# Optimization experiments

Hardware: AMD Instinct MI355X
Metric: run time of the kernel (lower is better)

Reference implementation:

```python
import jax, jax.numpy as jnp
import numpy as np

H = 12        # attention heads
BETA = 0.5    # blend weight between ctx-cosine probs and QK probs
LN_EPS = 1e-12


def layer_norm(x, g, b):
    mu = x.mean(-1, keepdims=True)
    var = ((x - mu) ** 2).mean(-1, keepdims=True)
    return (x - mu) * jax.lax.rsqrt(var + LN_EPS) * g + b


def setup_inputs() -> dict:
    key = jax.random.key(0)
    B, S, D, F, L = 16, 512, 768, 3072, 4
    ks = jax.random.split(key, 9)
    w = lambda k, shape: (jax.random.normal(k, shape, jnp.float32) * 0.02)
    return {
        "hidden_states": jax.random.normal(ks[0], (B, S, D), jnp.float32),
        "Wq": w(ks[1], (L, D, D)), "bq": jnp.zeros((L, D), jnp.float32),
        "Wk": w(ks[2], (L, D, D)), "bk": jnp.zeros((L, D), jnp.float32),
        "Wv": w(ks[3], (L, D, D)), "bv": jnp.zeros((L, D), jnp.float32),
        "Wc": w(ks[4], (L, D, D)), "bc": jnp.zeros((L, D), jnp.float32),
        "Wo": w(ks[5], (L, D, D)), "bo": jnp.zeros((L, D), jnp.float32),
        "g1": jnp.ones((L, D), jnp.float32), "b1": jnp.zeros((L, D), jnp.float32),
        "Wi": w(ks[6], (L, D, F)), "bi": jnp.zeros((L, F), jnp.float32),
        "Wo2": w(ks[7], (L, F, D)), "bo2": jnp.zeros((L, D), jnp.float32),
        "g2": jnp.ones((L, D), jnp.float32), "b2": jnp.zeros((L, D), jnp.float32),
    }


def reference(hidden_states, Wq, bq, Wk, bk, Wv, bv, Wc, bc, Wo, bo,
              g1, b1, Wi, bi, Wo2, bo2, g2, b2):
    B, S, D = hidden_states.shape
    Dh = D // H
    L = Wq.shape[0]
    eye = jnp.eye(S, dtype=hidden_states.dtype)
    scale = 1.0 / np.sqrt(Dh).astype(np.float32)

    def heads(t):  # [B,S,D] -> [B,H,S,Dh]
        return t.reshape(B, S, H, Dh).transpose(0, 2, 1, 3)

    x = hidden_states
    for i in range(L):  # small fixed layer loop
        q = heads(x @ Wq[i] + bq[i])
        k = heads(x @ Wk[i] + bk[i])
        v = heads(x @ Wv[i] + bv[i])
        c = heads(x @ Wc[i] + bc[i])

        # Branch 1: cosine-normalized context scores, flipped (1 - cos) + I
        cn = jnp.linalg.norm(c, axis=-1, keepdims=True)           # [B,H,S,1]
        denom = cn * jnp.swapaxes(cn, -1, -2)                     # [B,H,S,S]
        s1 = 1.0 - jnp.einsum('bhld,bhrd->bhlr', c, c) / denom + eye
        p1 = jax.nn.softmax(s1, axis=-1)

        # Branch 2: standard scaled QK scores
        s2 = jnp.einsum('bhld,bhrd->bhlr', q, k) * scale
        p2 = jax.nn.softmax(s2, axis=-1)

        p = BETA * p1 + (1.0 - BETA) * p2                          # beta blend
        ctx = jnp.einsum('bhlr,bhrd->bhld', p, v)                  # [B,H,S,Dh]
        ctx = ctx.transpose(0, 2, 1, 3).reshape(B, S, D)

        attn_out = layer_norm(ctx @ Wo[i] + bo[i] + x, g1[i], b1[i])
        h = jax.nn.gelu(attn_out @ Wi[i] + bi[i], approximate=False)
        x = layer_norm(h @ Wo2[i] + bo2[i] + attn_out, g2[i], b2[i])
    return x
```

## Files before the change

kernel.cpp:

```cpp
#include <hip/hip_runtime.h>
#include <math.h>

#define DD 768
#define FF 3072
#define SS 512
#define BB 16
#define NH 12
#define DH 64
#define NL 4
#define MM (BB*SS)

typedef __attribute__((ext_vector_type(8))) short short8;
typedef __attribute__((ext_vector_type(4))) float f32x4;

__device__ __forceinline__ unsigned short f2bf(float f) {
  unsigned u = __float_as_uint(f);
  return (unsigned short)((u + 0x7FFFu + ((u >> 16) & 1u)) >> 16);
}
__device__ __forceinline__ float bf2f(unsigned short s) {
  return __uint_as_float(((unsigned)s) << 16);
}

#define GLOAD_LDS(g, l) \
  __builtin_amdgcn_global_load_lds((const __attribute__((address_space(1))) void*)(g), \
                                   (__attribute__((address_space(3))) void*)(l), 16, 0, 0)

__global__ __launch_bounds__(256) void cvt_dual_k(const float* __restrict__ in,
                                                  float* __restrict__ outf,
                                                  unsigned short* __restrict__ outb, int n) {
  for (int i = blockIdx.x*256 + threadIdx.x; i < n; i += gridDim.x*256) {
    float v = in[i]; outf[i] = v; outb[i] = f2bf(v);
  }
}

__global__ __launch_bounds__(256) void tcvt_k(const float* __restrict__ src,
                                              unsigned short* __restrict__ dst,
                                              int K, int N) {
  __shared__ float t[32][33];
  const int n0 = blockIdx.x*32, k0 = blockIdx.y*32;
  const int tx = threadIdx.x & 31, ty = threadIdx.x >> 5;
#pragma unroll
  for (int i = 0; i < 32; i += 8)
    t[ty+i][tx] = src[(size_t)(k0+ty+i)*N + n0+tx];
  __syncthreads();
#pragma unroll
  for (int i = 0; i < 32; i += 8)
    dst[(size_t)(n0+ty+i)*K + k0+tx] = f2bf(t[tx][ty+i]);
}

__global__ __launch_bounds__(256) void tcvt5_k(const float* __restrict__ Wq,
                                               const float* __restrict__ Wk,
                                               const float* __restrict__ Wv,
                                               const float* __restrict__ Wc,
                                               const float* __restrict__ Wo,
                                               unsigned long long wD,
                                               unsigned short* __restrict__ WqkvcT,
                                               unsigned short* __restrict__ WoT) {
  __shared__ float t[32][33];
  const int z = blockIdx.z;
  const float* src = ((z == 0) ? Wq : (z == 1) ? Wk : (z == 2) ? Wv :
                      (z == 3) ? Wc : Wo) + wD;
  unsigned short* dst = (z < 4) ? (WqkvcT + (size_t)z*DD*DD) : WoT;
  const int n0 = blockIdx.x*32, k0 = blockIdx.y*32;
  const int tx = threadIdx.x & 31, ty = threadIdx.x >> 5;
#pragma unroll
  for (int i = 0; i < 32; i += 8)
    t[ty+i][tx] = src[(size_t)(k0+ty+i)*DD + n0+tx];
  __syncthreads();
#pragma unroll
  for (int i = 0; i < 32; i += 8)
    dst[(size_t)(n0+ty+i)*DD + k0+tx] = f2bf(t[tx][ty+i]);
}

__global__ __launch_bounds__(256) void bcat_k(const float* __restrict__ a,
                                              const float* __restrict__ b,
                                              const float* __restrict__ c,
                                              const float* __restrict__ d,
                                              float* __restrict__ out) {
  int i = blockIdx.x*256 + threadIdx.x;
  int w = i / 768;
  const float* s = (w == 0) ? a : (w == 1) ? b : (w == 2) ? c : d;
  out[i] = s[i - w*768];
}

template<int EPI, int OBF>
__global__ __launch_bounds__(256, 3) void mgemm_k(
    const unsigned short* __restrict__ A,
    const unsigned short* __restrict__ Bw,
    const float* __restrict__ bias,
    const float* __restrict__ resid,
    void* __restrict__ Cout, int M, int N, int K)
{
  __shared__ __align__(16) unsigned short As[2][128*32];
  __shared__ __align__(16) unsigned short Bs[2][128*32];
  const int nwg = gridDim.x * gridDim.y;
  int lin = blockIdx.y * gridDim.x + blockIdx.x;
  lin = (lin & 7) * (nwg >> 3) + (lin >> 3);
  const int bm = (lin / gridDim.x) * 128, bn = (lin % gridDim.x) * 128;
  const int tid = threadIdx.x;
  const int wave = tid >> 6, lane = tid & 63;
  const int wm = (wave >> 1)*64, wn = (wave & 1)*64;
  const int woff = wave*32*32;

  f32x4 acc[4][4] = {};

  const unsigned short* Ag = A  + (size_t)(bm + wave*32 + (lane>>2))*K + (lane&3)*8;
  const unsigned short* Bg = Bw + (size_t)(bn + wave*32 + (lane>>2))*K + (lane&3)*8;

  GLOAD_LDS(Ag,                As[0] + woff);
  GLOAD_LDS(Ag + 16*(size_t)K, As[0] + woff + 16*32);
  GLOAD_LDS(Bg,                Bs[0] + woff);
  GLOAD_LDS(Bg + 16*(size_t)K, Bs[0] + woff + 16*32);
  Ag += 32; Bg += 32;
  __syncthreads();

  const unsigned short* Ac = As[0]; unsigned short* An = As[1];
  const unsigned short* Bc = Bs[0]; unsigned short* Bn = Bs[1];
  const int nk = K >> 5;

#pragma unroll 1
  for (int t = 0; t < nk - 1; ++t) {
    GLOAD_LDS(Ag,                An + woff);
    GLOAD_LDS(Ag + 16*(size_t)K, An + woff + 16*32);
    GLOAD_LDS(Bg,                Bn + woff);
    GLOAD_LDS(Bg + 16*(size_t)K, Bn + woff + 16*32);
    Ag += 32; Bg += 32;

    short8 af[4], bfr[4];
#pragma unroll
    for (int i = 0; i < 4; ++i) {
      af[i]  = *(const short8*)&Ac[(wm + i*16 + (lane & 15))*32 + (lane >> 4)*8];
      bfr[i] = *(const short8*)&Bc[(wn + i*16 + (lane & 15))*32 + (lane >> 4)*8];
    }
    __builtin_amdgcn_s_setprio(1);
#pragma unroll
    for (int i = 0; i < 4; ++i)
#pragma unroll
      for (int j = 0; j < 4; ++j)
        acc[i][j] = __builtin_amdgcn_mfma_f32_16x16x32_bf16(af[i], bfr[j], acc[i][j], 0, 0, 0);
    __builtin_amdgcn_s_setprio(0);

    __syncthreads();
    const unsigned short* tA = Ac; Ac = An; An = (unsigned short*)tA;
    const unsigned short* tB = Bc; Bc = Bn; Bn = (unsigned short*)tB;
  }

  {
    short8 af[4], bfr[4];
#pragma unroll
    for (int i = 0; i < 4; ++i) {
      af[i]  = *(const short8*)&Ac[(wm + i*16 + (lane & 15))*32 + (lane >> 4)*8];
      bfr[i] = *(const short8*)&Bc[(wn + i*16 + (lane & 15))*32 + (lane >> 4)*8];
    }
#pragma unroll
    for (int i = 0; i < 4; ++i)
#pragma unroll
      for (int j = 0; j < 4; ++j)
        acc[i][j] = __builtin_amdgcn_mfma_f32_16x16x32_bf16(af[i], bfr[j], acc[i][j], 0, 0, 0);
  }

  const int col0 = bn + wn + (lane & 15);
  const int row0 = bm + wm + (lane >> 4)*4;
#pragma unroll
  for (int i = 0; i < 4; ++i) {
#pragma unroll
    for (int j = 0; j < 4; ++j) {
      const int n = col0 + j*16;
      const float bv = bias[n];
#pragma unroll
      for (int r = 0; r < 4; ++r) {
        const int m = row0 + i*16 + r;
        float v = acc[i][j][r] + bv;
        if (EPI == 1) v += resid[(size_t)m*N + n];
        if (EPI == 2) v = 0.5f*v*(1.0f + erff(v*0.70710678118654752f));
        if (OBF) ((unsigned short*)Cout)[(size_t)m*N + n] = f2bf(v);
        else     ((float*)Cout)[(size_t)m*N + n] = v;
      }
    }
  }
}

__global__ __launch_bounds__(256) void cnorm_k(const unsigned short* __restrict__ c,
                                               float* __restrict__ rn) {
  int idx = blockIdx.x*4 + (threadIdx.x >> 6);
  int lane = threadIdx.x & 63;
  int s  = idx % SS;
  int bh = idx / SS;
  int h  = bh % NH;
  int b  = bh / NH;
  float v = bf2f(c[((size_t)(b*SS + s))*FF + h*DH + lane]);
  float ss = v*v;
#pragma unroll
  for (int off = 32; off; off >>= 1) ss += __shfl_xor(ss, off, 64);
  if (lane == 0) rn[idx] = rsqrtf(ss);
}

__global__ __launch_bounds__(256) void vtrans_k(const unsigned short* __restrict__ v,
                                                unsigned short* __restrict__ VT) {
  __shared__ unsigned short t[64][72];
  const int s0 = blockIdx.x*64;
  const int h  = blockIdx.y;
  const int b  = blockIdx.z;
  const size_t base = (size_t)(b*SS)*FF + h*DH;
  const int row = threadIdx.x >> 2, seg = threadIdx.x & 3;
  const unsigned short* vg = v + base + (size_t)(s0+row)*FF + seg*16;
  *(uint4*)&t[row][seg*16]     = *(const uint4*)vg;
  *(uint4*)&t[row][seg*16 + 8] = *(const uint4*)(vg + 8);
  __syncthreads();
  unsigned short o[16];
#pragma unroll
  for (int u = 0; u < 16; ++u) o[u] = t[seg*16 + u][row];
  unsigned short* og = VT + ((size_t)(b*NH + h)*DH + row)*SS + s0 + seg*16;
  *(uint4*)og       = *(const uint4*)&o[0];
  *(uint4*)(og + 8) = *(const uint4*)&o[8];
}

__global__ __launch_bounds__(256, 3) void attn5_k(
    const unsigned short* __restrict__ q, const unsigned short* __restrict__ k,
    const unsigned short* __restrict__ c, const float* __restrict__ rn,
    const unsigned short* __restrict__ VT, unsigned short* __restrict__ ctxO)
{
  const int bid = blockIdx.x + 8*blockIdx.y + 96*blockIdx.z;
  const int l0  = ((bid >> 3) & 7) << 6;
  const int bh  = (bid & 7) + ((bid >> 6) << 3);
  const int h   = bh % NH;
  const int b   = bh / NH;
  const int tid = threadIdx.x;
  const int wave = tid >> 6, lane = tid & 63;
  const int wm = wave * 16;
  const int fr = lane & 15;
  const int fg = lane >> 4;
  const size_t base   = (size_t)(b*SS)*FF + h*DH;
  const size_t vtbase = (size_t)bh*DH*SS;

  __shared__ __align__(16) unsigned short Ks [2][64*72];
  __shared__ __align__(16) unsigned short Crs[2][64*72];
  __shared__ __align__(16) unsigned short Ps [4][16*72];
  unsigned short* Pw = Ps[wave];

  const unsigned short* qrow = q + base + (size_t)(l0 + wm + fr)*FF + fg*8;
  const unsigned short* crow = c + base + (size_t)(l0 + wm + fr)*FF + fg*8;
  const short8 aQ0 = *(const short8*)qrow;
  const short8 aQ1 = *(const short8*)(qrow + 32);
  const short8 aC0 = *(const short8*)crow;
  const short8 aC1 = *(const short8*)(crow + 32);

  float rnl[4];
#pragma unroll
  for (int reg = 0; reg < 4; ++reg)
    rnl[reg] = rn[(size_t)bh*SS + l0 + wm + fg*4 + reg];

  const int srow = tid >> 2, sseg = tid & 3;
  {
    const unsigned short* kg = k + base + (size_t)srow*FF + sseg*16;
    const unsigned short* cg = c + base + (size_t)srow*FF + sseg*16;
    *(uint4*)&Ks [0][srow*72 + sseg*16]     = *(const uint4*)kg;
    *(uint4*)&Ks [0][srow*72 + sseg*16 + 8] = *(const uint4*)(kg + 8);
    *(uint4*)&Crs[0][srow*72 + sseg*16]     = *(const uint4*)cg;
    *(uint4*)&Crs[0][srow*72 + sseg*16 + 8] = *(const uint4*)(cg + 8);
  }
  __syncthreads();

  float rs2[4], rs1[4];
#pragma unroll
  for (int r = 0; r < 4; ++r) { rs2[r] = 0.f; rs1[r] = 0.f; }
  f32x4 oc1[4] = {}, oc2[4] = {};

#pragma unroll 1
  for (int it = 0; it < 8; ++it) {
    const int r0 = it*64;
    const int cur = it & 1, nxt = cur ^ 1;

    uint4 nk0, nk1, nc0, nc1;
    if (it < 7) {
      const unsigned short* kg = k + base + (size_t)(r0 + 64 + srow)*FF + sseg*16;
      const unsigned short* cg = c + base + (size_t)(r0 + 64 + srow)*FF + sseg*16;
      nk0 = *(const uint4*)kg;  nk1 = *(const uint4*)(kg + 8);
      nc0 = *(const uint4*)cg;  nc1 = *(const uint4*)(cg + 8);
    }

    float rnr[4];
    short8 bv0[4], bv1[4];
#pragma unroll
    for (int nt = 0; nt < 4; ++nt) {
      rnr[nt] = rn[(size_t)bh*SS + r0 + nt*16 + fr];
      const unsigned short* vtr = VT + vtbase + (size_t)(nt*16 + fr)*SS + r0 + fg*8;
      bv0[nt] = *(const short8*)vtr;
      bv1[nt] = *(const short8*)(vtr + 32);
    }

    f32x4 s1a[4] = {}, s2a[4] = {};
#pragma unroll
    for (int nt = 0; nt < 4; ++nt) {
      const short8 bK0 = *(const short8*)&Ks [cur][(nt*16+fr)*72 + fg*8];
      const short8 bK1 = *(const short8*)&Ks [cur][(nt*16+fr)*72 + fg*8 + 32];
      const short8 bC0 = *(const short8*)&Crs[cur][(nt*16+fr)*72 + fg*8];
      const short8 bC1 = *(const short8*)&Crs[cur][(nt*16+fr)*72 + fg*8 + 32];
      s2a[nt] = __builtin_amdgcn_mfma_f32_16x16x32_bf16(aQ0, bK0, s2a[nt], 0,0,0);
      s2a[nt] = __builtin_amdgcn_mfma_f32_16x16x32_bf16(aQ1, bK1, s2a[nt], 0,0,0);
      s1a[nt] = __builtin_amdgcn_mfma_f32_16x16x32_bf16(aC0, bC0, s1a[nt], 0,0,0);
      s1a[nt] = __builtin_amdgcn_mfma_f32_16x16x32_bf16(aC1, bC1, s1a[nt], 0,0,0);
    }

    float sv1[4][4], sv2[4][4];
#pragma unroll
    for (int nt = 0; nt < 4; ++nt)
#pragma unroll
      for (int reg = 0; reg < 4; ++reg) {
        const int ql = wm + fg*4 + reg;
        const int rr = nt*16 + fr;
        sv2[reg][nt] = s2a[nt][reg] * 0.125f;
        sv1[reg][nt] = 1.0f - s1a[nt][reg]*rnl[reg]*rnr[nt]
                     + ((l0+ql) == (r0+rr) ? 1.0f : 0.0f);
      }

#pragma unroll
    for (int reg = 0; reg < 4; ++reg) {
      const int prow = (fg*4 + reg)*72;
#pragma unroll
      for (int nt = 0; nt < 4; ++nt) {
        const float x1 = __expf(sv1[reg][nt] - 3.0f);
        Pw[prow + nt*16 + fr] = f2bf(x1);
        rs1[reg] += x1;
      }
    }
    {
      const short8 p0 = *(const short8*)&Pw[fr*72 + fg*8];
      const short8 p1 = *(const short8*)&Pw[fr*72 + fg*8 + 32];
#pragma unroll
      for (int nt = 0; nt < 4; ++nt) {
        oc1[nt] = __builtin_amdgcn_mfma_f32_16x16x32_bf16(p0, bv0[nt], oc1[nt], 0,0,0);
        oc1[nt] = __builtin_amdgcn_mfma_f32_16x16x32_bf16(p1, bv1[nt], oc1[nt], 0,0,0);
      }
    }

#pragma unroll
    for (int reg = 0; reg < 4; ++reg) {
      const int prow = (fg*4 + reg)*72;
#pragma unroll
      for (int nt = 0; nt < 4; ++nt) {
        const float x2 = __expf(sv2[reg][nt] - 3.0f);
        Pw[prow + nt*16 + fr] = f2bf(x2);
        rs2[reg] += x2;
      }
    }
    {
      const short8 p0 = *(const short8*)&Pw[fr*72 + fg*8];
      const short8 p1 = *(const short8*)&Pw[fr*72 + fg*8 + 32];
#pragma unroll
      for (int nt = 0; nt < 4; ++nt) {
        oc2[nt] = __builtin_amdgcn_mfma_f32_16x16x32_bf16(p0, bv0[nt], oc2[nt], 0,0,0);
        oc2[nt] = __builtin_amdgcn_mfma_f32_16x16x32_bf16(p1, bv1[nt], oc2[nt], 0,0,0);
      }
    }

    if (it < 7) {
      *(uint4*)&Ks [nxt][srow*72 + sseg*16]     = nk0;
      *(uint4*)&Ks [nxt][srow*72 + sseg*16 + 8] = nk1;
      *(uint4*)&Crs[nxt][srow*72 + sseg*16]     = nc0;
      *(uint4*)&Crs[nxt][srow*72 + sseg*16 + 8] = nc1;
    }
    __syncthreads();
  }

#pragma unroll
  for (int reg = 0; reg < 4; ++reg) {
    float t1 = rs1[reg], t2 = rs2[reg];
#pragma unroll
    for (int off = 1; off < 16; off <<= 1) {
      t1 += __shfl_xor(t1, off, 64);
      t2 += __shfl_xor(t2, off, 64);
    }
    const float i1 = 0.5f / t1;
    const float i2 = 0.5f / t2;
    const int prow = (fg*4 + reg)*72;
#pragma unroll
    for (int nt = 0; nt < 4; ++nt)
      Pw[prow + nt*16 + fr] = f2bf(oc1[nt][reg]*i1 + oc2[nt][reg]*i2);
  }
  {
    const int row = lane >> 2, seg = lane & 3;
    const int Mrow = b*SS + l0 + wm + row;
    unsigned short* og = ctxO + (size_t)Mrow*DD + h*DH + seg*16;
    *(uint4*)og       = *(const uint4*)&Pw[row*72 + seg*16];
    *(uint4*)(og + 8) = *(const uint4*)&Pw[row*72 + seg*16 + 8];
  }
}

__global__ __launch_bounds__(256) void ln_k(const float* __restrict__ in,
                                            const float* __restrict__ g,
                                            const float* __restrict__ b,
                                            float* __restrict__ outf,
                                            unsigned short* __restrict__ outb) {
  __shared__ float xs[DD];
  __shared__ float red[8];
  const int tid = threadIdx.x;
  const float* xr = in + (size_t)blockIdx.x * DD;
  float* xo = outf + (size_t)blockIdx.x * DD;
  unsigned short* xbr = outb + (size_t)blockIdx.x * DD;
  float s = 0.f, s2 = 0.f;
  for (int d = tid; d < DD; d += 256) {
    float v = xr[d]; xs[d] = v; s += v; s2 += v*v;
  }
#pragma unroll
  for (int off = 32; off; off >>= 1) {
    s  += __shfl_xor(s,  off, 64);
    s2 += __shfl_xor(s2, off, 64);
  }
  if ((tid & 63) == 0) { red[tid >> 6] = s; red[4 + (tid >> 6)] = s2; }
  __syncthreads();
  const float mu  = (red[0]+red[1]+red[2]+red[3]) * (1.f/DD);
  const float ex2 = (red[4]+red[5]+red[6]+red[7]) * (1.f/DD);
  const float var = fmaxf(ex2 - mu*mu, 0.f);
  const float rstd = rsqrtf(var + 1e-12f);
  for (int d = tid; d < DD; d += 256) {
    float o = (xs[d]-mu)*rstd*g[d] + b[d];
    xo[d] = o;
    xbr[d] = f2bf(o);
  }
}

extern "C" void kernel_launch(void* const* d_in, const int* in_sizes, int n_in,
                              void* d_out, int out_size, void* d_ws, size_t ws_size,
                              hipStream_t stream) {
  const float* hs  = (const float*)d_in[0];
  const float* Wq  = (const float*)d_in[1];  const float* bq  = (const float*)d_in[2];
  const float* Wk  = (const float*)d_in[3];  const float* bk  = (const float*)d_in[4];
  const float* Wv  = (const float*)d_in[5];  const float* bv  = (const float*)d_in[6];
  const float* Wc  = (const float*)d_in[7];  const float* bc  = (const float*)d_in[8];
  const float* Wo  = (const float*)d_in[9];  const float* bo  = (const float*)d_in[10];
  const float* g1  = (const float*)d_in[11]; const float* b1  = (const float*)d_in[12];
  const float* Wi  = (const float*)d_in[13]; const float* bi  = (const float*)d_in[14];
  const float* Wo2 = (const float*)d_in[15]; const float* bo2 = (const float*)d_in[16];
  const float* g2  = (const float*)d_in[17]; const float* b2  = (const float*)d_in[18];

  const size_t XN  = (size_t)MM * DD;
  const size_t HN  = (size_t)MM * FF;
  const int    nBH = BB*NH*SS;
  const size_t WTN = 7667712;

  char* p = (char*)d_ws;
  float*          x      = (float*)p;           p += XN*4;
  float*          attnf  = (float*)p;           p += XN*4;
  unsigned short* qkvc16 = (unsigned short*)p;  p += HN*2;
  unsigned short* xb16   = (unsigned short*)p;  p += XN*2;
  unsigned short* ctx16  = (unsigned short*)p;  p += XN*2;
  unsigned short* attn16 = (unsigned short*)p;  p += XN*2;
  unsigned short* vt16   = (unsigned short*)p;  p += XN*2;
  unsigned short* WT     = (unsigned short*)p;  p += WTN*2;
  float*          bqkvc  = (float*)p;           p += 3072*4;
  float*          cnb    = (float*)p;           p += (size_t)nBH*4;
  const size_t need = (size_t)(p - (char*)d_ws);
  if (ws_size < need) return;

  unsigned short* WqkvcT = WT;
  unsigned short* WoT    = WT + 2359296;
  unsigned short* WiT    = WT + 2949120;
  unsigned short* Wo2T   = WT + 5308416;
  unsigned short* hb16   = qkvc16;

  cvt_dual_k<<<4096, 256, 0, stream>>>(hs, x, xb16, (int)XN);

  dim3 gGQ(FF/128, MM/128);
  dim3 gGD(DD/128, MM/128);
  dim3 gA(SS/64, NH, BB);
  dim3 t5(DD/32, DD/32, 5);
  dim3 tDF(FF/32, DD/32);
  dim3 tFD(DD/32, FF/32);

  for (int i = 0; i < NL; ++i) {
    const size_t wD = (size_t)i*DD*DD, wF = (size_t)i*DD*FF;
    tcvt5_k<<<t5, 256, 0, stream>>>(Wq, Wk, Wv, Wc, Wo, (unsigned long long)wD,
                                    WqkvcT, WoT);
    tcvt_k<<<tDF, 256, 0, stream>>>(Wi + wF, WiT,  DD, FF);
    tcvt_k<<<tFD, 256, 0, stream>>>(Wo2 + wF, Wo2T, FF, DD);
    bcat_k<<<12, 256, 0, stream>>>(bq + (size_t)i*DD, bk + (size_t)i*DD,
                                   bv + (size_t)i*DD, bc + (size_t)i*DD, bqkvc);

    mgemm_k<0,1><<<gGQ, 256, 0, stream>>>(xb16, WqkvcT, bqkvc, nullptr, qkvc16, MM, FF, DD);

    cnorm_k<<<nBH/4, 256, 0, stream>>>(qkvc16 + 2304, cnb);
    vtrans_k<<<gA, 256, 0, stream>>>(qkvc16 + 1536, vt16);
    attn5_k<<<gA, 256, 0, stream>>>(qkvc16, qkvc16 + 768, qkvc16 + 2304,
                                    cnb, vt16, ctx16);

    mgemm_k<1,0><<<gGD, 256, 0, stream>>>(ctx16, WoT, bo + (size_t)i*DD, x, attnf, MM, DD, DD);
    ln_k<<<MM, 256, 0, stream>>>(attnf, g1 + (size_t)i*DD, b1 + (size_t)i*DD, attnf, attn16);

    mgemm_k<2,1><<<gGQ, 256, 0, stream>>>(attn16, WiT, bi + (size_t)i*FF, nullptr, hb16, MM, FF, DD);
    mgemm_k<1,0><<<gGD, 256, 0, stream>>>(hb16, Wo2T, bo2 + (size_t)i*DD, attnf, x, MM, DD, FF);
    float* lnout = (i == NL-1) ? (float*)d_out : x;
    ln_k<<<MM, 256, 0, stream>>>(x, g2 + (size_t)i*DD, b2 + (size_t)i*DD, lnout, xb16);
  }
}
```

Baseline: 1.430 ms.

## Load K/C tiles directly into registers in attention, drop LDS staging

The attention kernel no longer stages K and C tiles through double-buffered shared memory with per-iteration barriers. Each wave now loads its MFMA B-operands straight from global memory, and the occupancy hint rises from 3 to 5 blocks per CU. The initial conversion also stops writing an fp32 copy of the input, and the first layer reads the residual from the original input. The aim is to cut LDS traffic and synchronisation, at the cost of redundant global/L2 reads of K and C across the four waves.

After: 2.385 ms. 66.9% more time.

```diff
diff --git a/kernel.cpp b/kernel.cpp
--- a/kernel.cpp
+++ b/kernel.cpp
@@ -25,12 +25,10 @@
   __builtin_amdgcn_global_load_lds((const __attribute__((address_space(1))) void*)(g), \
                                    (__attribute__((address_space(3))) void*)(l), 16, 0, 0)
 
-__global__ __launch_bounds__(256) void cvt_dual_k(const float* __restrict__ in,
-                                                  float* __restrict__ outf,
-                                                  unsigned short* __restrict__ outb, int n) {
-  for (int i = blockIdx.x*256 + threadIdx.x; i < n; i += gridDim.x*256) {
-    float v = in[i]; outf[i] = v; outb[i] = f2bf(v);
-  }
+__global__ __launch_bounds__(256) void cvt_k(const float* __restrict__ in,
+                                             unsigned short* __restrict__ outb, int n) {
+  for (int i = blockIdx.x*256 + threadIdx.x; i < n; i += gridDim.x*256)
+    outb[i] = f2bf(in[i]);
 }
 
 __global__ __launch_bounds__(256) void tcvt_k(const float* __restrict__ src,
@@ -215,7 +213,7 @@
   *(uint4*)(og + 8) = *(const uint4*)&o[8];
 }
 
-__global__ __launch_bounds__(256, 3) void attn5_k(
+__global__ __launch_bounds__(256, 5) void attn6_k(
     const unsigned short* __restrict__ q, const unsigned short* __restrict__ k,
     const unsigned short* __restrict__ c, const float* __restrict__ rn,
     const unsigned short* __restrict__ VT, unsigned short* __restrict__ ctxO)
@@ -233,9 +231,7 @@
   const size_t base   = (size_t)(b*SS)*FF + h*DH;
   const size_t vtbase = (size_t)bh*DH*SS;
 
-  __shared__ __align__(16) unsigned short Ks [2][64*72];
-  __shared__ __align__(16) unsigned short Crs[2][64*72];
-  __shared__ __align__(16) unsigned short Ps [4][16*72];
+  __shared__ __align__(16) unsigned short Ps[4][16*72];
   unsigned short* Pw = Ps[wave];
 
   const unsigned short* qrow = q + base + (size_t)(l0 + wm + fr)*FF + fg*8;
@@ -250,17 +246,6 @@
   for (int reg = 0; reg < 4; ++reg)
     rnl[reg] = rn[(size_t)bh*SS + l0 + wm + fg*4 + reg];
 
-  const int srow = tid >> 2, sseg = tid & 3;
-  {
-    const unsigned short* kg = k + base + (size_t)srow*FF + sseg*16;
-    const unsigned short* cg = c + base + (size_t)srow*FF + sseg*16;
-    *(uint4*)&Ks [0][srow*72 + sseg*16]     = *(const uint4*)kg;
-    *(uint4*)&Ks [0][srow*72 + sseg*16 + 8] = *(const uint4*)(kg + 8);
-    *(uint4*)&Crs[0][srow*72 + sseg*16]     = *(const uint4*)cg;
-    *(uint4*)&Crs[0][srow*72 + sseg*16 + 8] = *(const uint4*)(cg + 8);
-  }
-  __syncthreads();
-
   float rs2[4], rs1[4];
 #pragma unroll
   for (int r = 0; r < 4; ++r) { rs2[r] = 0.f; rs1[r] = 0.f; }
@@ -269,37 +254,30 @@
 #pragma unroll 1
   for (int it = 0; it < 8; ++it) {
     const int r0 = it*64;
-    const int cur = it & 1, nxt = cur ^ 1;
-
-    uint4 nk0, nk1, nc0, nc1;
-    if (it < 7) {
-      const unsigned short* kg = k + base + (size_t)(r0 + 64 + srow)*FF + sseg*16;
-      const unsigned short* cg = c + base + (size_t)(r0 + 64 + srow)*FF + sseg*16;
-      nk0 = *(const uint4*)kg;  nk1 = *(const uint4*)(kg + 8);
-      nc0 = *(const uint4*)cg;  nc1 = *(const uint4*)(cg + 8);
-    }
 
     float rnr[4];
-    short8 bv0[4], bv1[4];
+    short8 bv0[4], bv1[4], bK0[4], bK1[4], bC0[4], bC1[4];
 #pragma unroll
     for (int nt = 0; nt < 4; ++nt) {
       rnr[nt] = rn[(size_t)bh*SS + r0 + nt*16 + fr];
       const unsigned short* vtr = VT + vtbase + (size_t)(nt*16 + fr)*SS + r0 + fg*8;
       bv0[nt] = *(const short8*)vtr;
       bv1[nt] = *(const short8*)(vtr + 32);
+      const unsigned short* kr = k + base + (size_t)(r0 + nt*16 + fr)*FF + fg*8;
+      const unsigned short* cr = c + base + (size_t)(r0 + nt*16 + fr)*FF + fg*8;
+      bK0[nt] = *(const short8*)kr;
+      bK1[nt] = *(const short8*)(kr + 32);
+      bC0[nt] = *(const short8*)cr;
+      bC1[nt] = *(const short8*)(cr + 32);
     }
 
     f32x4 s1a[4] = {}, s2a[4] = {};
 #pragma unroll
     for (int nt = 0; nt < 4; ++nt) {
-      const short8 bK0 = *(const short8*)&Ks [cur][(nt*16+fr)*72 + fg*8];
-      const short8 bK1 = *(const short8*)&Ks [cur][(nt*16+fr)*72 + fg*8 + 32];
-      const short8 bC0 = *(const short8*)&Crs[cur][(nt*16+fr)*72 + fg*8];
-      const short8 bC1 = *(const short8*)&Crs[cur][(nt*16+fr)*72 + fg*8 + 32];
-      s2a[nt] = __builtin_amdgcn_mfma_f32_16x16x32_bf16(aQ0, bK0, s2a[nt], 0,0,0);
-      s2a[nt] = __builtin_amdgcn_mfma_f32_16x16x32_bf16(aQ1, bK1, s2a[nt], 0,0,0);
-      s1a[nt] = __builtin_amdgcn_mfma_f32_16x16x32_bf16(aC0, bC0, s1a[nt], 0,0,0);
-      s1a[nt] = __builtin_amdgcn_mfma_f32_16x16x32_bf16(aC1, bC1, s1a[nt], 0,0,0);
+      s2a[nt] = __builtin_amdgcn_mfma_f32_16x16x32_bf16(aQ0, bK0[nt], s2a[nt], 0,0,0);
+      s2a[nt] = __builtin_amdgcn_mfma_f32_16x16x32_bf16(aQ1, bK1[nt], s2a[nt], 0,0,0);
+      s1a[nt] = __builtin_amdgcn_mfma_f32_16x16x32_bf16(aC0, bC0[nt], s1a[nt], 0,0,0);
+      s1a[nt] = __builtin_amdgcn_mfma_f32_16x16x32_bf16(aC1, bC1[nt], s1a[nt], 0,0,0);
     }
 
     float sv1[4][4], sv2[4][4];
@@ -353,14 +331,6 @@
         oc2[nt] = __builtin_amdgcn_mfma_f32_16x16x32_bf16(p1, bv1[nt], oc2[nt], 0,0,0);
       }
     }
-
-    if (it < 7) {
-      *(uint4*)&Ks [nxt][srow*72 + sseg*16]     = nk0;
-      *(uint4*)&Ks [nxt][srow*72 + sseg*16 + 8] = nk1;
-      *(uint4*)&Crs[nxt][srow*72 + sseg*16]     = nc0;
-      *(uint4*)&Crs[nxt][srow*72 + sseg*16 + 8] = nc1;
-    }
-    __syncthreads();
   }
 
 #pragma unroll
@@ -459,7 +429,7 @@
   unsigned short* Wo2T   = WT + 5308416;
   unsigned short* hb16   = qkvc16;
 
-  cvt_dual_k<<<4096, 256, 0, stream>>>(hs, x, xb16, (int)XN);
+  cvt_k<<<4096, 256, 0, stream>>>(hs, xb16, (int)XN);
 
   dim3 gGQ(FF/128, MM/128);
   dim3 gGD(DD/128, MM/128);
@@ -481,10 +451,11 @@
 
     cnorm_k<<<nBH/4, 256, 0, stream>>>(qkvc16 + 2304, cnb);
     vtrans_k<<<gA, 256, 0, stream>>>(qkvc16 + 1536, vt16);
-    attn5_k<<<gA, 256, 0, stream>>>(qkvc16, qkvc16 + 768, qkvc16 + 2304,
+    attn6_k<<<gA, 256, 0, stream>>>(qkvc16, qkvc16 + 768, qkvc16 + 2304,
                                     cnb, vt16, ctx16);
 
-    mgemm_k<1,0><<<gGD, 256, 0, stream>>>(ctx16, WoT, bo + (size_t)i*DD, x, attnf, MM, DD, DD);
+    const float* res0 = (i == 0) ? hs : x;
+    mgemm_k<1,0><<<gGD, 256, 0, stream>>>(ctx16, WoT, bo + (size_t)i*DD, res0, attnf, MM, DD, DD);
     ln_k<<<MM, 256, 0, stream>>>(attnf, g1 + (size_t)i*DD, b1 + (size_t)i*DD, attnf, attn16);
 
     mgemm_k<2,1><<<gGQ, 256, 0, stream>>>(attn16, WiT, bi + (size_t)i*FF, nullptr, hb16, MM, FF, DD);
```
